# Performance work log

Measured on AMD Instinct MI355X. Metric: run time of the kernel, lower is better.

The kernel has to match this reference:

```python
import jax, jax.numpy as jnp
from jax import lax
import numpy as np

MAX_SELECT = 100
NMS_THRESH = 0.1
LINES_PER_BLOCK = 4
CHARS_PER_LINE = 1
BELONG_THRESH = 0.6
SCORE_THRESH = 0.1
SAMPLE_NUM = 10


def cxcywh_to_xyxy(b):
    cx, cy, w, h = jnp.split(b, 4, axis=-1)
    return jnp.concatenate([cx - 0.5 * w, cy - 0.5 * h, cx + 0.5 * w, cy + 0.5 * h], axis=-1)


def bezier_aabb(cp):
    # cp: [K, 8, 2] control points (two cubic beziers: top 0:4, bottom 4:8)
    t = jnp.linspace(0.0, 1.0, SAMPLE_NUM)[:, None]      # [S,1]
    ti = 1.0 - t
    basis = jnp.concatenate([ti ** 3, 3 * t * ti ** 2, 3 * t ** 2 * ti, t ** 3], axis=-1)  # [S,4]
    top = jnp.einsum('sf,kfd->ksd', basis, cp[:, 0:4, :])
    bot = jnp.einsum('sf,kfd->ksd', basis, cp[:, 4:8, :])
    pts = jnp.concatenate([top, bot], axis=1)            # [K, 2S, 2]
    return jnp.concatenate([pts.min(axis=1), pts.max(axis=1)], axis=-1)  # [K,4] = x1,y1,x2,y2


def nms_keep_mask(boxes, init_keep, thresh):
    # boxes already sorted by descending score (topk order); returns keep mask
    K = boxes.shape[0]
    area = (boxes[:, 2] - boxes[:, 0]) * (boxes[:, 3] - boxes[:, 1])
    tl = jnp.maximum(boxes[:, None, :2], boxes[None, :, :2])
    br = jnp.minimum(boxes[:, None, 2:], boxes[None, :, 2:])
    wh = jnp.clip(br - tl, 0.0)
    inter = wh[..., 0] * wh[..., 1]
    iou = inter / (area[:, None] + area[None, :] - inter)
    idx = jnp.arange(K)

    def body(keep, i):
        sup = (iou[i] > thresh) & (idx > i) & keep[i]
        return keep & ~sup, None

    keep, _ = lax.scan(body, init_keep, jnp.arange(K))
    return keep


def filter_image(probs, raw, tsize, parent_raw, ef, is_bezier):
    # probs: [N], raw: [N, 4 or 16], tsize: [2] = (h, w)
    img_h, img_w = tsize[0], tsize[1]
    scale_box = jnp.stack([img_w, img_h, img_w, img_h])
    K = MAX_SELECT
    vals, sidx = lax.top_k(probs, K)
    keep = vals > SCORE_THRESH
    keep = jnp.where(keep.any(), keep, jnp.arange(K) == 0)

    if is_bezier:
        scale_pts = jnp.tile(tsize, 8)                    # [h,w]*8, matches repeat(8)
        ctrl = (raw[sidx] * scale_pts).reshape(K, 8, 2)
        boxes = bezier_aabb(ctrl)
        data = ctrl
    else:
        data = cxcywh_to_xyxy(raw[sidx]) * scale_box
        boxes = data

    if parent_raw is not None:
        pbox = cxcywh_to_xyxy(parent_raw[sidx // ef]) * scale_box
        ix1 = jnp.maximum(boxes[:, 0], pbox[:, 0])
        iy1 = jnp.maximum(boxes[:, 1], pbox[:, 1])
        ix2 = jnp.minimum(boxes[:, 2], pbox[:, 2])
        iy2 = jnp.minimum(boxes[:, 3], pbox[:, 3])
        inter = jnp.clip(ix2 - ix1, 0.0) * jnp.clip(iy2 - iy1, 0.0)
        carea = (boxes[:, 2] - boxes[:, 0]) * (boxes[:, 3] - boxes[:, 1])
        belong = inter / (carea + 1e-6)
        valid = belong > BELONG_THRESH
        fb = jnp.arange(K) == jnp.argmax(jnp.where(keep, belong, -jnp.inf))
        valid = jnp.where((valid & keep).any(), valid, fb)
        mask = keep & valid
    else:
        maxs = jnp.stack([img_w, img_h, img_w, img_h])
        data = jnp.clip(data, 0.0, maxs)
        boxes = data
        mask = keep

    nk = nms_keep_mask(lax.stop_gradient(boxes), mask, NMS_THRESH)
    if is_bezier:
        data = data.reshape(K, 16)
    data = jnp.where(nk[:, None], data, 0.0)
    scores = jnp.where(nk, vals, 0.0)
    return data, scores, nk


def _probs(logits):
    return jax.nn.sigmoid(logits)[..., 0]


def reference(pred_block_logits, pred_line_logits, pred_char_logits,
              pred_block, pred_line, pred_char, target_sizes):
    bp = _probs(pred_block_logits)
    lp = _probs(pred_line_logits)
    cp = _probs(pred_char_logits)
    blk = jax.vmap(lambda p, r, t: filter_image(p, r, t, None, 1, False))(bp, pred_block, target_sizes)
    lin = jax.vmap(lambda p, r, pr, t: filter_image(p, r, t, pr, LINES_PER_BLOCK, False))(lp, pred_line, pred_block, target_sizes)
    chr_ = jax.vmap(lambda p, r, pr, t: filter_image(p, r, t, pr, CHARS_PER_LINE, True))(cp, pred_char, pred_line, target_sizes)
    # padded outputs: (data, scores, keep_mask) per level; invalid rows are zeroed
    return (*blk, *lin, *chr_)


def setup_inputs() -> dict:
    key = jax.random.key(0)
    ks = jax.random.split(key, 7)
    B, NB, NL, NC = 64, 4096, 16384, 16384
    return {
        'pred_block_logits': jax.random.normal(ks[0], (B, NB, 1), jnp.float32),
        'pred_line_logits': jax.random.normal(ks[1], (B, NL, 1), jnp.float32),
        'pred_char_logits': jax.random.normal(ks[2], (B, NC, 1), jnp.float32),
        'pred_block': jax.random.uniform(ks[3], (B, NB, 4), jnp.float32),
        'pred_line': jax.random.uniform(ks[4], (B, NL, 4), jnp.float32),
        'pred_char': jax.random.uniform(ks[5], (B, NC, 16), jnp.float32),
        'target_sizes': 512.0 + 1024.0 * jax.random.uniform(ks[6], (B, 2), jnp.float32),
    }
```

## Files before the change

kernel.cpp:

```cpp
#include <hip/hip_runtime.h>
#include <math.h>

#define NTHREADS 1024
#define NWAVES 16
#define KSEL 100
#define NBINS 2048
#define CAP 1024
#define SCORE_TH 0.1f
#define NMS_TH 0.1f
#define BELONG_TH 0.6f

typedef unsigned long long ull;

__device__ __forceinline__ ull make_key(float f, unsigned gidx) {
    unsigned u = __float_as_uint(f);
    u = (u & 0x80000000u) ? ~u : (u | 0x80000000u);
    return (((ull)u) << 32) | (ull)(0xFFFFFFFFu - gidx);
}
__device__ __forceinline__ float key_val(ull k) {
    unsigned u = (unsigned)(k >> 32);
    u = (u & 0x80000000u) ? (u ^ 0x80000000u) : ~u;
    return __uint_as_float(u);
}
__device__ __forceinline__ unsigned key_idx(ull k) {
    return 0xFFFFFFFFu - (unsigned)(k & 0xFFFFFFFFu);
}
__device__ __forceinline__ int binof(float p) {
    int b = (int)(p * (float)NBINS);
    b = b < 0 ? 0 : (b > NBINS - 1 ? NBINS - 1 : b);
    return b;
}
__device__ __forceinline__ unsigned gidx_of(int e, int tid) {
    return ((unsigned)(e >> 2)) * (NTHREADS * 4) + ((unsigned)tid << 2) + (unsigned)(e & 3);
}

struct SharedMem {
    union {
        unsigned hist[NBINS];
        ull cand[CAP];
        ull part[NWAVES];
    } u;
    int bstar;
    int scnt;
    int wsum[NWAVES];
    float prob[KSEL];
    int   sidx[KSEL];
    alignas(16) float box[KSEL][4];
    float data16[KSEL][16];
    float area[KSEL];
    float belong[KSEL];
    ull nmsrow[KSEL][2];
    unsigned char keep[KSEL];
    unsigned char valid[KSEL];
    unsigned char nk[KSEL];
    int argm;
    int anyvk;
};

template <int NPT, bool IS_BEZIER, bool HAS_PARENT>
__device__ void filter_impl(SharedMem* sm,
                            const float* __restrict__ logits,
                            const float* __restrict__ raw,
                            const float* __restrict__ parent_raw,
                            const float* __restrict__ tsizes,
                            float* __restrict__ out_data,
                            float* __restrict__ out_scores,
                            float* __restrict__ out_keep,
                            int img, int N, int PN, int ef) {
    const int tid = threadIdx.x;
    const int lane = tid & 63;
    const int wv = tid >> 6;
    const float* lg = logits + (size_t)img * N;

#pragma unroll
    for (int i = tid; i < NBINS; i += NTHREADS) sm->u.hist[i] = 0;
    if (tid == 0) sm->scnt = 0;
    __syncthreads();

    float p[NPT];
    const float4* lg4 = (const float4*)lg;
#pragma unroll
    for (int v = 0; v < NPT / 4; ++v) {
        float4 x = lg4[v * NTHREADS + tid];
        p[4 * v + 0] = 1.0f / (1.0f + expf(-x.x));
        p[4 * v + 1] = 1.0f / (1.0f + expf(-x.y));
        p[4 * v + 2] = 1.0f / (1.0f + expf(-x.z));
        p[4 * v + 3] = 1.0f / (1.0f + expf(-x.w));
    }

#pragma unroll
    for (int j = 0; j < NPT; ++j)
        atomicAdd(&sm->u.hist[binof(p[j])], 1u);
    __syncthreads();

    int c0 = (int)sm->u.hist[NBINS - 1 - 2 * tid];
    int c1 = (int)sm->u.hist[NBINS - 2 - 2 * tid];
    int s = c0 + c1;
    int vv = s;
#pragma unroll
    for (int off = 1; off < 64; off <<= 1) {
        int o = __shfl_up(vv, off, 64);
        if (lane >= off) vv += o;
    }
    if (lane == 63) sm->wsum[wv] = vv;
    __syncthreads();
    int base = 0;
#pragma unroll
    for (int u2 = 0; u2 < NWAVES; ++u2) base += (u2 < wv) ? sm->wsum[u2] : 0;
    int run = base + vv - s;
    if (run < KSEL && run + c0 >= KSEL) sm->bstar = NBINS - 1 - 2 * tid;
    int run2 = run + c0;
    if (run2 < KSEL && run2 + c1 >= KSEL) sm->bstar = NBINS - 2 - 2 * tid;
    __syncthreads();
    const int bstar = sm->bstar;

#pragma unroll
    for (int j = 0; j < NPT; ++j) {
        if (binof(p[j]) >= bstar) {
            int pos = atomicAdd(&sm->scnt, 1);
            if (pos < CAP) sm->u.cand[pos] = make_key(p[j], gidx_of(j, tid));
        }
    }
    __syncthreads();
    const int cnt = sm->scnt;

    if (cnt <= CAP) {
        for (int t = tid; t < cnt; t += NTHREADS) {
            ull mk = sm->u.cand[t];
            int rank = 0;
            for (int u2 = 0; u2 < cnt; ++u2) rank += (sm->u.cand[u2] > mk) ? 1 : 0;
            if (rank < KSEL) {
                sm->prob[rank] = key_val(mk);
                sm->sidx[rank] = (int)key_idx(mk);
            }
        }
    } else {
        ull best = make_key(p[0], gidx_of(0, tid));
#pragma unroll
        for (int j = 1; j < NPT; ++j) {
            ull kk = make_key(p[j], gidx_of(j, tid));
            if (kk > best) best = kk;
        }
        for (int k = 0; k < KSEL; ++k) {
            ull m = best;
#pragma unroll
            for (int off = 32; off > 0; off >>= 1) {
                ull o = __shfl_down(m, off, 64);
                if (o > m) m = o;
            }
            if (lane == 0) sm->u.part[wv] = m;
            __syncthreads();
            ull w = sm->u.part[0];
#pragma unroll
            for (int q = 1; q < NWAVES; ++q)
                if (sm->u.part[q] > w) w = sm->u.part[q];
            if (tid == 0) {
                sm->prob[k] = key_val(w);
                sm->sidx[k] = (int)key_idx(w);
            }
            __syncthreads();
            unsigned gidx = key_idx(w);
            if (((gidx >> 2) & (NTHREADS - 1)) == (unsigned)tid) {
                int e = (int)(((gidx >> 12) << 2) | (gidx & 3));
#pragma unroll
                for (int jj = 0; jj < NPT; ++jj)
                    if (jj == e) p[jj] = -INFINITY;
                best = make_key(p[0], gidx_of(0, tid));
#pragma unroll
                for (int jj = 1; jj < NPT; ++jj) {
                    ull kk = make_key(p[jj], gidx_of(jj, tid));
                    if (kk > best) best = kk;
                }
            }
        }
    }
    __syncthreads();

    const float Himg = tsizes[img * 2 + 0];
    const float Wimg = tsizes[img * 2 + 1];

    if (tid < KSEL) {
        const int k = tid;
        const int si = sm->sidx[k];
        const float val = sm->prob[k];
        const bool any = sm->prob[0] > SCORE_TH;
        bool keep = any ? (val > SCORE_TH) : (k == 0);

        float bx1, by1, bx2, by2;
        if (IS_BEZIER) {
            const float4* r4 = (const float4*)(raw + ((size_t)img * N + si) * 16);
            float c16[16];
#pragma unroll
            for (int v = 0; v < 4; ++v) {
                float4 x = r4[v];
                c16[4 * v + 0] = x.x * Himg;
                c16[4 * v + 1] = x.y * Wimg;
                c16[4 * v + 2] = x.z * Himg;
                c16[4 * v + 3] = x.w * Wimg;
            }
            float mn0 = INFINITY, mn1 = INFINITY, mx0 = -INFINITY, mx1 = -INFINITY;
            const float step = 1.0f / 9.0f;
#pragma unroll
            for (int sNum = 0; sNum < 10; ++sNum) {
                float t = (float)sNum * step;
                float ti = 1.0f - t;
                float b0 = ti * ti * ti;
                float b1 = 3.0f * t * ti * ti;
                float b2 = 3.0f * t * t * ti;
                float b3 = t * t * t;
#pragma unroll
                for (int cu = 0; cu < 2; ++cu) {
                    const float* cc = c16 + cu * 8;
                    float p0 = b0 * cc[0] + b1 * cc[2] + b2 * cc[4] + b3 * cc[6];
                    float p1 = b0 * cc[1] + b1 * cc[3] + b2 * cc[5] + b3 * cc[7];
                    mn0 = fminf(mn0, p0); mx0 = fmaxf(mx0, p0);
                    mn1 = fminf(mn1, p1); mx1 = fmaxf(mx1, p1);
                }
            }
            bx1 = mn0; by1 = mn1; bx2 = mx0; by2 = mx1;
#pragma unroll
            for (int mm = 0; mm < 16; ++mm) sm->data16[k][mm] = c16[mm];
        } else {
            float4 r = *(const float4*)(raw + ((size_t)img * N + si) * 4);
            float cx = r.x, cy = r.y, w = r.z, h = r.w;
            bx1 = (cx - 0.5f * w) * Wimg;
            by1 = (cy - 0.5f * h) * Himg;
            bx2 = (cx + 0.5f * w) * Wimg;
            by2 = (cy + 0.5f * h) * Himg;
            if (!HAS_PARENT) {
                bx1 = fminf(fmaxf(bx1, 0.0f), Wimg);
                by1 = fminf(fmaxf(by1, 0.0f), Himg);
                bx2 = fminf(fmaxf(bx2, 0.0f), Wimg);
                by2 = fminf(fmaxf(by2, 0.0f), Himg);
            }
        }
        sm->box[k][0] = bx1; sm->box[k][1] = by1;
        sm->box[k][2] = bx2; sm->box[k][3] = by2;
        sm->area[k] = (bx2 - bx1) * (by2 - by1);
        sm->keep[k] = keep ? 1 : 0;

        if (HAS_PARENT) {
            int pi = si / ef;
            float4 pr = *(const float4*)(parent_raw + ((size_t)img * PN + pi) * 4);
            float px1 = (pr.x - 0.5f * pr.z) * Wimg;
            float py1 = (pr.y - 0.5f * pr.w) * Himg;
            float px2 = (pr.x + 0.5f * pr.z) * Wimg;
            float py2 = (pr.y + 0.5f * pr.w) * Himg;
            float ix1 = fmaxf(bx1, px1), iy1 = fmaxf(by1, py1);
            float ix2 = fminf(bx2, px2), iy2 = fminf(by2, py2);
            float inter = fmaxf(ix2 - ix1, 0.0f) * fmaxf(iy2 - iy1, 0.0f);
            float carea = (bx2 - bx1) * (by2 - by1);
            float belong = inter / (carea + 1e-6f);
            sm->belong[k] = belong;
            sm->valid[k] = (belong > BELONG_TH) ? 1 : 0;
        }
    }
    __syncthreads();

    if (HAS_PARENT) {
        if (tid < 64) {
            ull k0 = make_key(sm->keep[tid] ? sm->belong[tid] : -INFINITY, (unsigned)tid);
            bool p0 = sm->valid[tid] && sm->keep[tid];
            ull k1 = 0;
            bool p1 = false;
            if (tid < KSEL - 64) {
                k1 = make_key(sm->keep[tid + 64] ? sm->belong[tid + 64] : -INFINITY,
                              (unsigned)(tid + 64));
                p1 = sm->valid[tid + 64] && sm->keep[tid + 64];
            }
            ull m = k0 > k1 ? k0 : k1;
#pragma unroll
            for (int off = 32; off > 0; off >>= 1) {
                ull o = __shfl_xor(m, off, 64);
                if (o > m) m = o;
            }
            ull bal = __ballot(p0 || p1);
            if (lane == 0) {
                sm->argm = (int)key_idx(m);
                sm->anyvk = (bal != 0ULL) ? 1 : 0;
            }
        }
        __syncthreads();
        if (tid < KSEL) {
            bool valid = sm->anyvk ? (sm->valid[tid] != 0) : (tid == sm->argm);
            sm->nk[tid] = (sm->keep[tid] && valid) ? 1 : 0;
        }
    } else {
        if (tid < KSEL) sm->nk[tid] = sm->keep[tid];
    }
    __syncthreads();

    {
        float4 b0 = *(const float4*)sm->box[lane];
        float a0 = sm->area[lane];
        float4 b1 = make_float4(0.f, 0.f, 0.f, 0.f);
        float a1 = 0.f;
        if (lane < KSEL - 64) {
            b1 = *(const float4*)sm->box[lane + 64];
            a1 = sm->area[lane + 64];
        }
        for (int i = wv; i < KSEL; i += NWAVES) {
            float rx1, ry1, rx2, ry2, ra;
            if (i < 64) {
                rx1 = __shfl(b0.x, i, 64); ry1 = __shfl(b0.y, i, 64);
                rx2 = __shfl(b0.z, i, 64); ry2 = __shfl(b0.w, i, 64);
                ra  = __shfl(a0, i, 64);
            } else {
                rx1 = __shfl(b1.x, i - 64, 64); ry1 = __shfl(b1.y, i - 64, 64);
                rx2 = __shfl(b1.z, i - 64, 64); ry2 = __shfl(b1.w, i - 64, 64);
                ra  = __shfl(a1, i - 64, 64);
            }
            float ix1 = fmaxf(rx1, b0.x), iy1 = fmaxf(ry1, b0.y);
            float ix2 = fminf(rx2, b0.z), iy2 = fminf(ry2, b0.w);
            float in0 = fmaxf(ix2 - ix1, 0.0f) * fmaxf(iy2 - iy1, 0.0f);
            float iou0 = in0 / (ra + a0 - in0);
            bool sup0 = (lane > i) && (iou0 > NMS_TH);
            float jx1 = fmaxf(rx1, b1.x), jy1 = fmaxf(ry1, b1.y);
            float jx2 = fminf(rx2, b1.z), jy2 = fminf(ry2, b1.w);
            float in1 = fmaxf(jx2 - jx1, 0.0f) * fmaxf(jy2 - jy1, 0.0f);
            float iou1 = in1 / (ra + a1 - in1);
            bool sup1 = (lane < KSEL - 64) && ((lane + 64) > i) && (iou1 > NMS_TH);
            ull w0 = __ballot(sup0);
            ull w1 = __ballot(sup1);
            if (lane == 0) { sm->nmsrow[i][0] = w0; sm->nmsrow[i][1] = w1; }
        }
    }
    __syncthreads();

    if (tid < 64) {
        const int l = lane;
        ull r0lo = sm->nmsrow[l][0], r0hi = sm->nmsrow[l][1];
        ull r1lo = 0, r1hi = 0;
        if (l < KSEL - 64) { r1lo = sm->nmsrow[l + 64][0]; r1hi = sm->nmsrow[l + 64][1]; }
        ull keepLo = __ballot(sm->nk[l] != 0);
        ull keepHi = __ballot((l < KSEL - 64) && (sm->nk[l + 64] != 0));
#pragma unroll
        for (int i = 0; i < KSEL; ++i) {
            bool ki = (i < 64) ? (((keepLo >> i) & 1ULL) != 0)
                               : (((keepHi >> (i - 64)) & 1ULL) != 0);
            ull slo = (i < 64) ? __shfl(r0lo, i, 64) : __shfl(r1lo, i - 64, 64);
            ull shi = (i < 64) ? __shfl(r0hi, i, 64) : __shfl(r1hi, i - 64, 64);
            keepLo &= ki ? ~slo : ~0ULL;
            keepHi &= ki ? ~shi : ~0ULL;
        }
        sm->nk[l] = (unsigned char)((keepLo >> l) & 1ULL);
        if (l < KSEL - 64) sm->nk[l + 64] = (unsigned char)((keepHi >> l) & 1ULL);
    }
    __syncthreads();

    if (tid < KSEL) {
        const int k = tid;
        const bool nk = sm->nk[k] != 0;
        out_scores[(size_t)img * KSEL + k] = nk ? sm->prob[k] : 0.0f;
        out_keep[(size_t)img * KSEL + k] = nk ? 1.0f : 0.0f;
        if (IS_BEZIER) {
#pragma unroll
            for (int mm = 0; mm < 16; ++mm)
                out_data[((size_t)img * KSEL + k) * 16 + mm] = nk ? sm->data16[k][mm] : 0.0f;
        } else {
#pragma unroll
            for (int mm = 0; mm < 4; ++mm)
                out_data[((size_t)img * KSEL + k) * 4 + mm] = nk ? sm->box[k][mm] : 0.0f;
        }
    }
}

__global__ __launch_bounds__(NTHREADS) void postprocess_kernel(
    const float* __restrict__ blk_logits, const float* __restrict__ lin_logits,
    const float* __restrict__ chr_logits, const float* __restrict__ blk_raw,
    const float* __restrict__ lin_raw, const float* __restrict__ chr_raw,
    const float* __restrict__ tsizes, float* __restrict__ out) {
    __shared__ SharedMem sm;
    const int b = blockIdx.x;
    const int level = b >> 6;
    const int img = b & 63;

    float* blk_data = out + 0;
    float* blk_sc   = out + 25600;
    float* blk_kp   = out + 32000;
    float* lin_data = out + 38400;
    float* lin_sc   = out + 64000;
    float* lin_kp   = out + 70400;
    float* chr_data = out + 76800;
    float* chr_sc   = out + 179200;
    float* chr_kp   = out + 185600;

    if (level == 0) {
        filter_impl<4, false, false>(&sm, blk_logits, blk_raw, nullptr, tsizes,
                                     blk_data, blk_sc, blk_kp, img, 4096, 0, 1);
    } else if (level == 1) {
        filter_impl<16, false, true>(&sm, lin_logits, lin_raw, blk_raw, tsizes,
                                     lin_data, lin_sc, lin_kp, img, 16384, 4096, 4);
    } else {
        filter_impl<16, true, true>(&sm, chr_logits, chr_raw, lin_raw, tsizes,
                                    chr_data, chr_sc, chr_kp, img, 16384, 16384, 1);
    }
}

extern "C" void kernel_launch(void* const* d_in, const int* in_sizes, int n_in,
                              void* d_out, int out_size, void* d_ws, size_t ws_size,
                              hipStream_t stream) {
    (void)in_sizes; (void)n_in; (void)d_ws; (void)ws_size; (void)out_size;
    const float* blk_logits = (const float*)d_in[0];
    const float* lin_logits = (const float*)d_in[1];
    const float* chr_logits = (const float*)d_in[2];
    const float* blk_raw = (const float*)d_in[3];
    const float* lin_raw = (const float*)d_in[4];
    const float* chr_raw = (const float*)d_in[5];
    const float* tsz = (const float*)d_in[6];
    float* out = (float*)d_out;

    hipLaunchKernelGGL(postprocess_kernel, dim3(192), dim3(NTHREADS), 0, stream,
                       blk_logits, lin_logits, chr_logits, blk_raw, lin_raw,
                       chr_raw, tsz, out);
}
```

Before: 131.8 us.

## Recompute sigmoid from global instead of holding probs in registers; sparse NMS loop

Drops the per-thread register array of probabilities. Sigmoids are recomputed by reloading the logits in the histogram, candidate-gather and fallback top-k passes, which lowers register pressure. The fallback iterative selection now rescans all elements below the previous maximum each round instead of patching a register array. The NMS resolution loop walks only the surviving kept indices using ctz instead of a fixed 100-step unrolled loop. The trade-off is extra global/L2 reads and repeated exp work in exchange for fewer registers and a shorter serial NMS chain.

```diff
diff --git a/kernel.cpp b/kernel.cpp
--- a/kernel.cpp
+++ b/kernel.cpp
@@ -25,13 +25,13 @@
 __device__ __forceinline__ unsigned key_idx(ull k) {
     return 0xFFFFFFFFu - (unsigned)(k & 0xFFFFFFFFu);
 }
+__device__ __forceinline__ float sigmoidf(float x) {
+    return 1.0f / (1.0f + expf(-x));
+}
 __device__ __forceinline__ int binof(float p) {
     int b = (int)(p * (float)NBINS);
     b = b < 0 ? 0 : (b > NBINS - 1 ? NBINS - 1 : b);
     return b;
-}
-__device__ __forceinline__ unsigned gidx_of(int e, int tid) {
-    return ((unsigned)(e >> 2)) * (NTHREADS * 4) + ((unsigned)tid << 2) + (unsigned)(e & 3);
 }
 
 struct SharedMem {
@@ -71,26 +71,21 @@
     const int lane = tid & 63;
     const int wv = tid >> 6;
     const float* lg = logits + (size_t)img * N;
+    const float4* lg4 = (const float4*)lg;
 
 #pragma unroll
     for (int i = tid; i < NBINS; i += NTHREADS) sm->u.hist[i] = 0;
     if (tid == 0) sm->scnt = 0;
     __syncthreads();
 
-    float p[NPT];
-    const float4* lg4 = (const float4*)lg;
 #pragma unroll
     for (int v = 0; v < NPT / 4; ++v) {
         float4 x = lg4[v * NTHREADS + tid];
-        p[4 * v + 0] = 1.0f / (1.0f + expf(-x.x));
-        p[4 * v + 1] = 1.0f / (1.0f + expf(-x.y));
-        p[4 * v + 2] = 1.0f / (1.0f + expf(-x.z));
-        p[4 * v + 3] = 1.0f / (1.0f + expf(-x.w));
-    }
-
-#pragma unroll
-    for (int j = 0; j < NPT; ++j)
-        atomicAdd(&sm->u.hist[binof(p[j])], 1u);
+        atomicAdd(&sm->u.hist[binof(sigmoidf(x.x))], 1u);
+        atomicAdd(&sm->u.hist[binof(sigmoidf(x.y))], 1u);
+        atomicAdd(&sm->u.hist[binof(sigmoidf(x.z))], 1u);
+        atomicAdd(&sm->u.hist[binof(sigmoidf(x.w))], 1u);
+    }
     __syncthreads();
 
     int c0 = (int)sm->u.hist[NBINS - 1 - 2 * tid];
@@ -115,10 +110,16 @@
     const int bstar = sm->bstar;
 
 #pragma unroll
-    for (int j = 0; j < NPT; ++j) {
-        if (binof(p[j]) >= bstar) {
-            int pos = atomicAdd(&sm->scnt, 1);
-            if (pos < CAP) sm->u.cand[pos] = make_key(p[j], gidx_of(j, tid));
+    for (int v = 0; v < NPT / 4; ++v) {
+        float4 x = lg4[v * NTHREADS + tid];
+        float q[4] = {sigmoidf(x.x), sigmoidf(x.y), sigmoidf(x.z), sigmoidf(x.w)};
+#pragma unroll
+        for (int j = 0; j < 4; ++j) {
+            if (binof(q[j]) >= bstar) {
+                int pos = atomicAdd(&sm->scnt, 1);
+                unsigned gidx = (unsigned)(v * (NTHREADS * 4) + tid * 4 + j);
+                if (pos < CAP) sm->u.cand[pos] = make_key(q[j], gidx);
+            }
         }
     }
     __syncthreads();
@@ -134,47 +135,40 @@
                 sm->sidx[rank] = (int)key_idx(mk);
             }
         }
+        __syncthreads();
     } else {
-        ull best = make_key(p[0], gidx_of(0, tid));
-#pragma unroll
-        for (int j = 1; j < NPT; ++j) {
-            ull kk = make_key(p[j], gidx_of(j, tid));
-            if (kk > best) best = kk;
-        }
+        ull prev = ~0ULL;
         for (int k = 0; k < KSEL; ++k) {
-            ull m = best;
+            ull best = 0;
+#pragma unroll
+            for (int v = 0; v < NPT / 4; ++v) {
+                float4 x = lg4[v * NTHREADS + tid];
+                float q[4] = {sigmoidf(x.x), sigmoidf(x.y), sigmoidf(x.z), sigmoidf(x.w)};
+#pragma unroll
+                for (int j = 0; j < 4; ++j) {
+                    ull kk = make_key(q[j], (unsigned)(v * (NTHREADS * 4) + tid * 4 + j));
+                    if (kk < prev && kk > best) best = kk;
+                }
+            }
 #pragma unroll
             for (int off = 32; off > 0; off >>= 1) {
-                ull o = __shfl_down(m, off, 64);
-                if (o > m) m = o;
-            }
-            if (lane == 0) sm->u.part[wv] = m;
+                ull o = __shfl_down(best, off, 64);
+                if (o > best) best = o;
+            }
+            if (lane == 0) sm->u.part[wv] = best;
             __syncthreads();
             ull w = sm->u.part[0];
 #pragma unroll
-            for (int q = 1; q < NWAVES; ++q)
-                if (sm->u.part[q] > w) w = sm->u.part[q];
+            for (int q2 = 1; q2 < NWAVES; ++q2)
+                if (sm->u.part[q2] > w) w = sm->u.part[q2];
             if (tid == 0) {
                 sm->prob[k] = key_val(w);
                 sm->sidx[k] = (int)key_idx(w);
             }
+            prev = w;
             __syncthreads();
-            unsigned gidx = key_idx(w);
-            if (((gidx >> 2) & (NTHREADS - 1)) == (unsigned)tid) {
-                int e = (int)(((gidx >> 12) << 2) | (gidx & 3));
-#pragma unroll
-                for (int jj = 0; jj < NPT; ++jj)
-                    if (jj == e) p[jj] = -INFINITY;
-                best = make_key(p[0], gidx_of(0, tid));
-#pragma unroll
-                for (int jj = 1; jj < NPT; ++jj) {
-                    ull kk = make_key(p[jj], gidx_of(jj, tid));
-                    if (kk > best) best = kk;
-                }
-            }
-        }
-    }
-    __syncthreads();
+        }
+    }
 
     const float Himg = tsizes[img * 2 + 0];
     const float Wimg = tsizes[img * 2 + 1];
@@ -330,18 +324,29 @@
     if (tid < 64) {
         const int l = lane;
         ull r0lo = sm->nmsrow[l][0], r0hi = sm->nmsrow[l][1];
-        ull r1lo = 0, r1hi = 0;
-        if (l < KSEL - 64) { r1lo = sm->nmsrow[l + 64][0]; r1hi = sm->nmsrow[l + 64][1]; }
+        ull r1hi = 0;
+        if (l < KSEL - 64) r1hi = sm->nmsrow[l + 64][1];
         ull keepLo = __ballot(sm->nk[l] != 0);
         ull keepHi = __ballot((l < KSEL - 64) && (sm->nk[l + 64] != 0));
-#pragma unroll
-        for (int i = 0; i < KSEL; ++i) {
-            bool ki = (i < 64) ? (((keepLo >> i) & 1ULL) != 0)
-                               : (((keepHi >> (i - 64)) & 1ULL) != 0);
-            ull slo = (i < 64) ? __shfl(r0lo, i, 64) : __shfl(r1lo, i - 64, 64);
-            ull shi = (i < 64) ? __shfl(r0hi, i, 64) : __shfl(r1hi, i - 64, 64);
-            keepLo &= ki ? ~slo : ~0ULL;
-            keepHi &= ki ? ~shi : ~0ULL;
+        ull remLo = keepLo, remHi = keepHi;
+        while (remLo | remHi) {
+            if (remLo) {
+                int i = __builtin_ctzll(remLo);
+                ull slo = __shfl(r0lo, i, 64);
+                ull shi = __shfl(r0hi, i, 64);
+                keepLo &= ~slo;
+                keepHi &= ~shi;
+                ull gt = (i >= 63) ? 0ULL : (~0ULL << (i + 1));
+                remLo = keepLo & gt;
+                remHi = keepHi;
+            } else {
+                int i = __builtin_ctzll(remHi);
+                ull shi = __shfl(r1hi, i, 64);
+                keepHi &= ~shi;
+                ull gt = (i >= 63) ? 0ULL : (~0ULL << (i + 1));
+                remHi = keepHi & gt;
+                remLo = 0;
+            }
         }
         sm->nk[l] = (unsigned char)((keepLo >> l) & 1ULL);
         if (l < KSEL - 64) sm->nk[l + 64] = (unsigned char)((keepHi >> l) & 1ULL);
```

Result: no change. 130.1 us (-1.3%).
